# Performance work log

Measured on AMD Instinct MI355X. Metric: run time of the kernel, lower is better.

The kernel has to match this reference:

```python
import jax, jax.numpy as jnp
import numpy as np

B_, S, D_IN, D_OUT = 4, 2048, 4096, 4096
N, RANK, ALPHA = 8, 16, 32
SCALE = ALPHA / RANK


def setup_inputs() -> dict:
    key = jax.random.key(0)
    kx, ka, kb, kw, kbias = jax.random.split(key, 5)
    x = jax.random.normal(kx, (B_, S, D_IN), dtype=jnp.float32)
    # lora_A.weight: [rank, in_features]; lora_B.weight: [out_features, rank]
    lora_A = jax.random.normal(ka, (N, RANK, D_IN), dtype=jnp.float32) * (1.0 / np.sqrt(D_IN))
    lora_B = jax.random.normal(kb, (N, D_OUT, RANK), dtype=jnp.float32) * (1.0 / np.sqrt(RANK))
    W = jax.random.normal(kw, (D_OUT, D_IN), dtype=jnp.float32) * (1.0 / np.sqrt(D_IN))
    bias = jax.random.normal(kbias, (D_OUT,), dtype=jnp.float32) * 0.01
    lora_weights = jnp.full((N,), 1.0 / N, dtype=jnp.float32)  # param_weight init
    return {"x": x, "lora_A": lora_A, "lora_B": lora_B, "W": W,
            "bias": bias, "lora_weights": lora_weights}


def reference(x, lora_A, lora_B, W, bias, lora_weights):
    # Dropout(p=0.01) treated as identity (eval mode) for deterministic reference.
    # low-rank projections for all adapters at once: [n, b, s, r]
    h = jnp.einsum('bsd,nrd->nbsr', x, lora_A)
    # up-projection with per-adapter scale * learned weight fused into B
    coef = (SCALE * lora_weights)[:, None, None]           # [n,1,1]
    lora_out = jnp.einsum('nbsr,nor->bso', h, lora_B * coef)
    base = jnp.einsum('bsd,od->bso', x, W) + bias
    return base + lora_out
```

## Files before the change

### kernel.cpp

```cpp
#include <hip/hip_runtime.h>
#include <hip/hip_bf16.h>
#include <stdint.h>


typedef __attribute__((ext_vector_type(4))) float f32x4;
typedef __attribute__((ext_vector_type(8))) __bf16 bf16x8;
typedef __attribute__((ext_vector_type(8))) unsigned short u16x8;

#define GLOBAL_AS(p) ((const __attribute__((address_space(1))) void*)(p))
#define LDS_AS(p)    ((__attribute__((address_space(3))) void*)(p))

__device__ __forceinline__ ushort f2b(float f) {
    __hip_bfloat16 h = __float2bfloat16(f);
    ushort u;
    __builtin_memcpy(&u, &h, 2);
    return u;
}

__global__ __launch_bounds__(256) void prep_a_kernel(const float* __restrict__ lA,
                                                     ushort* __restrict__ AcatT) {
    __shared__ ushort tile[64][136];
    const int tid = threadIdx.x;
    const int d0 = blockIdx.x * 64;
#pragma unroll
    for (int it = 0; it < 32; ++it) {
        int k = it * 4 + (tid >> 6);
        int dc = tid & 63;
        tile[dc][k] = f2b(lA[(size_t)k * 4096 + d0 + dc]);
    }
    __syncthreads();
#pragma unroll
    for (int it = 0; it < 4; ++it) {
        int g = it * 256 + tid;
        int dc = g >> 4, slot = g & 15;
        u16x8 v;
#pragma unroll
        for (int e = 0; e < 8; ++e) v[e] = tile[dc][slot * 8 + e];
        *reinterpret_cast<u16x8*>(&AcatT[((size_t)(d0 + dc)) * 128 + slot * 8]) = v;
    }
}

__global__ void prep_b_kernel(const float* __restrict__ lB,
                              const float* __restrict__ lw,
                              ushort* __restrict__ Bcat)
{
    int idx = blockIdx.x * 256 + threadIdx.x;
    int o = idx >> 7, k = idx & 127;
    int n = k >> 4, r = k & 15;
    Bcat[idx] = f2b(2.0f * lw[n] * lB[((size_t)n * 4096 + o) * 16 + r]);
}

__global__ void cvtx_kernel(const float* __restrict__ x, ushort* __restrict__ xb) {
    size_t i = ((size_t)blockIdx.x * 256 + threadIdx.x) * 8;
    const float4* xf = (const float4*)(x + i);
    float4 a = xf[0], b = xf[1];
    u16x8 r;
    r[0] = f2b(a.x); r[1] = f2b(a.y); r[2] = f2b(a.z); r[3] = f2b(a.w);
    r[4] = f2b(b.x); r[5] = f2b(b.y); r[6] = f2b(b.z); r[7] = f2b(b.w);
    *reinterpret_cast<u16x8*>(xb + i) = r;
}

template <bool OUT_F32, bool ADD_BIAS, bool ADD_C>
__global__ __launch_bounds__(256) void gemm_bt(
    const ushort* __restrict__ Amat, const ushort* __restrict__ Bmat,
    const float* __restrict__ aux, void* __restrict__ OutP,
    int M, int N, int K)
{
    constexpr int BK = 32;
    __shared__ __align__(16) ushort As[2 * 128 * BK];
    __shared__ __align__(16) ushort Bs[2 * 128 * BK];

    const int tid  = threadIdx.x;
    const int lane = tid & 63;
    const int w    = tid >> 6;
    const int wm   = (w >> 1) * 64;
    const int wn   = (w & 1) * 64;
    const int quad = lane >> 4;
    const int lrow = lane & 15;
    const int m0 = blockIdx.x * 128;
    const int n0 = blockIdx.y * 128;

    const int srow = (w * 2) * 16 + (lane >> 2);
    const int kofs = (lane & 3) * 8;
    const ushort* agp0 = Amat + (size_t)(m0 + srow) * K + kofs;
    const ushort* agp1 = agp0 + (size_t)16 * K;
    const ushort* bgp0 = Bmat + (size_t)(n0 + srow) * K + kofs;
    const ushort* bgp1 = bgp0 + (size_t)16 * K;
    ushort* lA00 = &As[(w * 2) * 512];
    ushort* lA01 = &As[(w * 2 + 1) * 512];
    ushort* lB00 = &Bs[(w * 2) * 512];
    ushort* lB01 = &Bs[(w * 2 + 1) * 512];

    f32x4 acc[4][4] = {};
    const int nK = K >> 6;
    for (int kt = 0; kt < nK; ++kt) {
        __syncthreads();
        __builtin_amdgcn_global_load_lds(GLOBAL_AS(agp0),      LDS_AS(lA00),        16, 0, 0);
        __builtin_amdgcn_global_load_lds(GLOBAL_AS(agp1),      LDS_AS(lA01),        16, 0, 0);
        __builtin_amdgcn_global_load_lds(GLOBAL_AS(agp0 + 32), LDS_AS(lA00 + 4096), 16, 0, 0);
        __builtin_amdgcn_global_load_lds(GLOBAL_AS(agp1 + 32), LDS_AS(lA01 + 4096), 16, 0, 0);
        __builtin_amdgcn_global_load_lds(GLOBAL_AS(bgp0),      LDS_AS(lB00),        16, 0, 0);
        __builtin_amdgcn_global_load_lds(GLOBAL_AS(bgp1),      LDS_AS(lB01),        16, 0, 0);
        __builtin_amdgcn_global_load_lds(GLOBAL_AS(bgp0 + 32), LDS_AS(lB00 + 4096), 16, 0, 0);
        __builtin_amdgcn_global_load_lds(GLOBAL_AS(bgp1 + 32), LDS_AS(lB01 + 4096), 16, 0, 0);
        agp0 += 64; agp1 += 64; bgp0 += 64; bgp1 += 64;
        __syncthreads();

#pragma unroll
        for (int h = 0; h < 2; ++h) {
            const ushort* ab = &As[h * 4096];
            const ushort* bb = &Bs[h * 4096];
            bf16x8 af[4], bfr[4];
#pragma unroll
            for (int i = 0; i < 4; ++i)
                af[i] = *reinterpret_cast<const bf16x8*>(&ab[(wm + i * 16 + lrow) * BK + quad * 8]);
#pragma unroll
            for (int j = 0; j < 4; ++j)
                bfr[j] = *reinterpret_cast<const bf16x8*>(&bb[(wn + j * 16 + lrow) * BK + quad * 8]);
#pragma unroll
            for (int i = 0; i < 4; ++i)
#pragma unroll
                for (int j = 0; j < 4; ++j)
                    acc[i][j] = __builtin_amdgcn_mfma_f32_16x16x32_bf16(af[i], bfr[j], acc[i][j], 0, 0, 0);
        }
    }

#pragma unroll
    for (int i = 0; i < 4; ++i) {
        const int row = m0 + wm + i * 16 + quad * 4;
#pragma unroll
        for (int j = 0; j < 4; ++j) {
            const int col = n0 + wn + j * 16 + lrow;
            float badd = ADD_BIAS ? aux[col] : 0.0f;
#pragma unroll
            for (int v = 0; v < 4; ++v) {
                float val = acc[i][j][v] + badd;
                if (ADD_C) val += aux[(size_t)(row + v) * N + col];
                if (OUT_F32)
                    ((float*)OutP)[(size_t)(row + v) * N + col] = val;
                else
                    ((ushort*)OutP)[(size_t)(row + v) * N + col] = f2b(val);
            }
        }
    }
}

__global__ __launch_bounds__(256) void gemm_af32(
    const float* __restrict__ Af, const ushort* __restrict__ Bmat,
    const float* __restrict__ bias, float* __restrict__ Out,
    int M, int N, int K)
{
    constexpr int BM = 128, BN = 128, BK = 32;
    __shared__ __align__(16) ushort As[BM * BK];
    __shared__ __align__(16) ushort Bs[BN * BK];

    const int tid  = threadIdx.x;
    const int lane = tid & 63;
    const int w    = tid >> 6;
    const int wm   = (w >> 1) * 64;
    const int wn   = (w & 1) * 64;
    const int quad = lane >> 4;
    const int lrow = lane & 15;
    const int m0 = blockIdx.x * BM;
    const int n0 = blockIdx.y * BN;

    const int srow = (w * 2) * 16 + (lane >> 2);
    const int kofs = (lane & 3) * 8;
    const ushort* bgp0 = Bmat + (size_t)(n0 + srow) * K + kofs;
    const ushort* bgp1 = bgp0 + (size_t)16 * K;
    ushort* lB0 = &Bs[(w * 2) * 512];
    ushort* lB1 = &Bs[(w * 2 + 1) * 512];

    f32x4 acc[4][4] = {};
    const int nK = K / BK;
    for (int kt = 0; kt < nK; ++kt) {
        __syncthreads();
        __builtin_amdgcn_global_load_lds(GLOBAL_AS(bgp0), LDS_AS(lB0), 16, 0, 0);
        __builtin_amdgcn_global_load_lds(GLOBAL_AS(bgp1), LDS_AS(lB1), 16, 0, 0);
        bgp0 += BK; bgp1 += BK;
#pragma unroll
        for (int gg = 0; gg < 2; ++gg) {
            int g = tid + gg * 256;
            int row = g >> 2, kc = (g & 3) * 8;
            const float* src = Af + (size_t)(m0 + row) * K + (size_t)kt * BK + kc;
            float4 a = *(const float4*)src;
            float4 b = *(const float4*)(src + 4);
            u16x8 r;
            r[0] = f2b(a.x); r[1] = f2b(a.y); r[2] = f2b(a.z); r[3] = f2b(a.w);
            r[4] = f2b(b.x); r[5] = f2b(b.y); r[6] = f2b(b.z); r[7] = f2b(b.w);
            *reinterpret_cast<u16x8*>(&As[row * BK + kc]) = r;
        }
        __syncthreads();

        bf16x8 af[4], bfr[4];
#pragma unroll
        for (int i = 0; i < 4; ++i)
            af[i] = *reinterpret_cast<const bf16x8*>(&As[(wm + i * 16 + lrow) * BK + quad * 8]);
#pragma unroll
        for (int j = 0; j < 4; ++j)
            bfr[j] = *reinterpret_cast<const bf16x8*>(&Bs[(wn + j * 16 + lrow) * BK + quad * 8]);
#pragma unroll
        for (int i = 0; i < 4; ++i)
#pragma unroll
            for (int j = 0; j < 4; ++j)
                acc[i][j] = __builtin_amdgcn_mfma_f32_16x16x32_bf16(af[i], bfr[j], acc[i][j], 0, 0, 0);
    }

#pragma unroll
    for (int i = 0; i < 4; ++i) {
        const int row = m0 + wm + i * 16 + quad * 4;
#pragma unroll
        for (int j = 0; j < 4; ++j) {
            const int col = n0 + wn + j * 16 + lrow;
            float badd = bias[col];
#pragma unroll
            for (int v = 0; v < 4; ++v)
                Out[(size_t)(row + v) * N + col] = acc[i][j][v] + badd;
        }
    }
}

__global__ void naive_kernel(const float* __restrict__ x, const float* __restrict__ lA,
                             const float* __restrict__ lB, const float* __restrict__ W,
                             const float* __restrict__ bias, const float* __restrict__ lw,
                             float* __restrict__ out)
{
    __shared__ float xs[4096];
    __shared__ float h[128];
    const int m = blockIdx.x;
    for (int d = threadIdx.x; d < 4096; d += 256)
        xs[d] = x[(size_t)m * 4096 + d];
    __syncthreads();
    for (int k = threadIdx.x; k < 128; k += 256) {
        const float* arow = lA + (size_t)k * 4096;
        float s = 0.f;
        for (int d = 0; d < 4096; ++d) s += xs[d] * arow[d];
        h[k] = s;
    }
    __syncthreads();
    for (int o = threadIdx.x; o < 4096; o += 256) {
        const float* wrow = W + (size_t)o * 4096;
        float s = bias[o];
        for (int d = 0; d < 4096; ++d) s += xs[d] * wrow[d];
        for (int n = 0; n < 8; ++n) {
            const float* brow = lB + ((size_t)n * 4096 + o) * 16;
            float t = 0.f;
            for (int r = 0; r < 16; ++r) t += h[n * 16 + r] * brow[r];
            s += 2.0f * lw[n] * t;
        }
        out[(size_t)m * 4096 + o] = s;
    }
}

extern "C" void kernel_launch(void* const* d_in, const int* in_sizes, int n_in,
                              void* d_out, int out_size, void* d_ws, size_t ws_size,
                              hipStream_t stream)
{
    const float* x    = (const float*)d_in[0];
    const float* lA   = (const float*)d_in[1];
    const float* lB   = (const float*)d_in[2];
    const float* W    = (const float*)d_in[3];
    const float* bias = (const float*)d_in[4];
    const float* lw   = (const float*)d_in[5];
    float* out = (float*)d_out;

    ushort* Bcat  = (ushort*)d_ws;
    ushort* AcatT = Bcat + (size_t)4096 * 128;
    ushort* Weff  = AcatT + (size_t)4096 * 128;
    ushort* xb    = Weff + (size_t)4096 * 4096;
    const size_t need_t2 = (2 * (size_t)4096 * 128 + (size_t)4096 * 4096) * 2;
    const size_t need_t1 = need_t2 + (size_t)8192 * 4096 * 2;

    if (ws_size >= need_t2) {
        prep_a_kernel<<<64, 256, 0, stream>>>(lA, AcatT);
        prep_b_kernel<<<2048, 256, 0, stream>>>(lB, lw, Bcat);
        gemm_bt<false, false, true><<<dim3(32, 32), 256, 0, stream>>>(
            Bcat, AcatT, W, Weff, 4096, 4096, 128);
        if (ws_size >= need_t1) {
            cvtx_kernel<<<16384, 256, 0, stream>>>(x, xb);
            gemm_bt<true, true, false><<<dim3(64, 32), 256, 0, stream>>>(
                xb, Weff, bias, out, 8192, 4096, 4096);
        } else {
            gemm_af32<<<dim3(64, 32), 256, 0, stream>>>(
                x, Weff, bias, out, 8192, 4096, 4096);
        }
    } else {
        naive_kernel<<<8192, 256, 0, stream>>>(x, lA, lB, W, bias, lw, out);
    }
}
```

Before: 651.5 us.

## Replace main bf16 GEMM with 256x256-tile pipelined kernel using direct global-to-LDS loads

Swaps the 128x128 gemm_bt used for the dominant x·Weff product for a new 512-thread kernel computing 256x256 output tiles. It double-buffers LDS via global_load_lds, swizzles LDS columns to avoid bank conflicts, interleaves quarter-tile loads with MFMA groups using barriers and setprio, and remaps block ids for L2 locality. The larger tile raises arithmetic intensity and overlaps memory with compute, at the cost of heavy register use (128 accumulators) and hand-tuned waitcnt logic that depends on the exact dimensions.

```diff
diff --git a/kernel.cpp b/kernel.cpp
--- a/kernel.cpp
+++ b/kernel.cpp
@@ -145,6 +145,156 @@
     }
 }
 
+__global__ __launch_bounds__(512, 2) void gemm256_bias(
+    const ushort* __restrict__ Amat, const ushort* __restrict__ Bmat,
+    const float* __restrict__ bias, float* __restrict__ Out,
+    int M, int N, int K)
+{
+    __shared__ __align__(16) ushort As[2][2][128 * 64];
+    __shared__ __align__(16) ushort Bs[2][2][128 * 64];
+
+    const int tid  = threadIdx.x;
+    const int l    = tid & 63;
+    const int w    = tid >> 6;
+    const int wr   = w >> 2;
+    const int wc   = w & 3;
+    const int quad = l >> 4;
+    const int lrow = l & 15;
+
+    const int nbn = N >> 8;
+    const int cpx = gridDim.x >> 3;
+    int id = ((int)blockIdx.x & 7) * cpx + ((int)blockIdx.x >> 3);
+    const int m0 = (id / nbn) * 256;
+    const int n0 = (id % nbn) * 256;
+
+    const int cOff = ((l & 7) * 8) ^ (((l >> 5) & 1) << 4);
+    const ushort* aBase = Amat + (size_t)(m0 + (w * 2) * 8 + (l >> 3)) * K + cOff;
+    const ushort* bBase = Bmat + (size_t)(n0 + (w * 2) * 8 + (l >> 3)) * K + cOff;
+    const int dC = 8 * K;
+    const int dH = 128 * K;
+    const int st0 = w * 1024;
+    const int st1 = w * 1024 + 512;
+
+    const int aRow0 = wr * 64 + lrow;
+    const int bCol0 = wc * 32 + lrow;
+    const int kqf = ((lrow >> 2) & 1) << 4;
+    const int kq0 = (quad * 8) ^ kqf;
+    const int kq1 = (32 + quad * 8) ^ kqf;
+
+    f32x4 acc[8][4] = {};
+    bf16x8 af[4][2], bf[2][2];
+
+    const int nT = K >> 6;
+
+#define GLDS(gp, lp) __builtin_amdgcn_global_load_lds(GLOBAL_AS(gp), LDS_AS(lp), 16, 0, 0)
+
+#define LOAD_AF(cur_, half_) do { \
+    af[0][0] = *reinterpret_cast<const bf16x8*>(&As[cur_][half_][(aRow0 +  0) * 64 + kq0]); \
+    af[0][1] = *reinterpret_cast<const bf16x8*>(&As[cur_][half_][(aRow0 +  0) * 64 + kq1]); \
+    af[1][0] = *reinterpret_cast<const bf16x8*>(&As[cur_][half_][(aRow0 + 16) * 64 + kq0]); \
+    af[1][1] = *reinterpret_cast<const bf16x8*>(&As[cur_][half_][(aRow0 + 16) * 64 + kq1]); \
+    af[2][0] = *reinterpret_cast<const bf16x8*>(&As[cur_][half_][(aRow0 + 32) * 64 + kq0]); \
+    af[2][1] = *reinterpret_cast<const bf16x8*>(&As[cur_][half_][(aRow0 + 32) * 64 + kq1]); \
+    af[3][0] = *reinterpret_cast<const bf16x8*>(&As[cur_][half_][(aRow0 + 48) * 64 + kq0]); \
+    af[3][1] = *reinterpret_cast<const bf16x8*>(&As[cur_][half_][(aRow0 + 48) * 64 + kq1]); \
+} while (0)
+
+#define LOAD_BF(cur_, half_) do { \
+    bf[0][0] = *reinterpret_cast<const bf16x8*>(&Bs[cur_][half_][(bCol0 +  0) * 64 + kq0]); \
+    bf[0][1] = *reinterpret_cast<const bf16x8*>(&Bs[cur_][half_][(bCol0 +  0) * 64 + kq1]); \
+    bf[1][0] = *reinterpret_cast<const bf16x8*>(&Bs[cur_][half_][(bCol0 + 16) * 64 + kq0]); \
+    bf[1][1] = *reinterpret_cast<const bf16x8*>(&Bs[cur_][half_][(bCol0 + 16) * 64 + kq1]); \
+} while (0)
+
+#define MFMA1(qm_, qn_, i_, j_, kh_) \
+    acc[(qm_) * 4 + (i_)][(qn_) * 2 + (j_)] = __builtin_amdgcn_mfma_f32_16x16x32_bf16( \
+        af[i_][kh_], bf[j_][kh_], acc[(qm_) * 4 + (i_)][(qn_) * 2 + (j_)], 0, 0, 0)
+
+#define MFMA_QUAD(qm_, qn_) do { \
+    MFMA1(qm_,qn_,0,0,0); MFMA1(qm_,qn_,0,1,0); MFMA1(qm_,qn_,1,0,0); MFMA1(qm_,qn_,1,1,0); \
+    MFMA1(qm_,qn_,2,0,0); MFMA1(qm_,qn_,2,1,0); MFMA1(qm_,qn_,3,0,0); MFMA1(qm_,qn_,3,1,0); \
+    MFMA1(qm_,qn_,0,0,1); MFMA1(qm_,qn_,0,1,1); MFMA1(qm_,qn_,1,0,1); MFMA1(qm_,qn_,1,1,1); \
+    MFMA1(qm_,qn_,2,0,1); MFMA1(qm_,qn_,2,1,1); MFMA1(qm_,qn_,3,0,1); MFMA1(qm_,qn_,3,1,1); \
+} while (0)
+
+#define BAR_MID() do { \
+    asm volatile("" ::: "memory"); \
+    __builtin_amdgcn_s_barrier(); \
+    __builtin_amdgcn_sched_barrier(0); \
+    asm volatile("s_waitcnt lgkmcnt(0)" ::: "memory"); \
+    __builtin_amdgcn_sched_barrier(0); \
+    __builtin_amdgcn_s_setprio(1); \
+} while (0)
+
+#define BAR_END() do { \
+    __builtin_amdgcn_s_setprio(0); \
+    asm volatile("" ::: "memory"); \
+    __builtin_amdgcn_s_barrier(); \
+    __builtin_amdgcn_sched_barrier(0); \
+} while (0)
+
+#define VGUARD() asm volatile("s_waitcnt vmcnt(4)" ::: "memory")
+
+#define TILE_STEP(cur_, nxt_, tt_) do { \
+    const int ks = ((tt_) + 1) << 6; \
+    const bool doSt = ((tt_) + 1) < nT; \
+     \
+    LOAD_AF(cur_, 0); LOAD_BF(cur_, 0); \
+    if (doSt) { GLDS(aBase + ks, &As[nxt_][0][st0]); GLDS(aBase + dC + ks, &As[nxt_][0][st1]); } \
+    BAR_MID(); MFMA_QUAD(0, 0); VGUARD(); BAR_END(); \
+     \
+    LOAD_BF(cur_, 1); \
+    if (doSt) { GLDS(bBase + ks, &Bs[nxt_][0][st0]); GLDS(bBase + dC + ks, &Bs[nxt_][0][st1]); } \
+    BAR_MID(); MFMA_QUAD(0, 1); VGUARD(); BAR_END(); \
+     \
+    LOAD_AF(cur_, 1); \
+    if (doSt) { GLDS(bBase + dH + ks, &Bs[nxt_][1][st0]); GLDS(bBase + dH + dC + ks, &Bs[nxt_][1][st1]); } \
+    BAR_MID(); MFMA_QUAD(1, 1); BAR_END(); \
+     \
+    LOAD_BF(cur_, 0); \
+    if (doSt) { GLDS(aBase + dH + ks, &As[nxt_][1][st0]); GLDS(aBase + dH + dC + ks, &As[nxt_][1][st1]); } \
+    BAR_MID(); MFMA_QUAD(1, 0); VGUARD(); BAR_END(); \
+} while (0)
+
+    GLDS(aBase,           &As[0][0][st0]); GLDS(aBase + dC,      &As[0][0][st1]);
+    GLDS(bBase,           &Bs[0][0][st0]); GLDS(bBase + dC,      &Bs[0][0][st1]);
+    GLDS(bBase + dH,      &Bs[0][1][st0]); GLDS(bBase + dH + dC, &Bs[0][1][st1]);
+    GLDS(aBase + dH,      &As[0][1][st0]); GLDS(aBase + dH + dC, &As[0][1][st1]);
+    asm volatile("s_waitcnt vmcnt(4)" ::: "memory");
+    asm volatile("" ::: "memory");
+    __builtin_amdgcn_s_barrier();
+    __builtin_amdgcn_sched_barrier(0);
+
+#pragma unroll 1
+    for (int t = 0; t < nT; t += 2) {
+        TILE_STEP(0, 1, t);
+        TILE_STEP(1, 0, t + 1);
+    }
+
+#pragma unroll
+    for (int i = 0; i < 8; ++i) {
+        const int row = m0 + (i >> 2) * 128 + wr * 64 + (i & 3) * 16 + quad * 4;
+#pragma unroll
+        for (int j = 0; j < 4; ++j) {
+            const int col = n0 + (j >> 1) * 128 + wc * 32 + (j & 1) * 16 + lrow;
+            const float badd = bias[col];
+#pragma unroll
+            for (int v = 0; v < 4; ++v)
+                Out[(size_t)(row + v) * N + col] = acc[i][j][v] + badd;
+        }
+    }
+
+#undef GLDS
+#undef LOAD_AF
+#undef LOAD_BF
+#undef MFMA1
+#undef MFMA_QUAD
+#undef BAR_MID
+#undef BAR_END
+#undef VGUARD
+#undef TILE_STEP
+}
+
 __global__ __launch_bounds__(256) void gemm_af32(
     const float* __restrict__ Af, const ushort* __restrict__ Bmat,
     const float* __restrict__ bias, float* __restrict__ Out,
@@ -278,7 +428,7 @@
             Bcat, AcatT, W, Weff, 4096, 4096, 128);
         if (ws_size >= need_t1) {
             cvtx_kernel<<<16384, 256, 0, stream>>>(x, xb);
-            gemm_bt<true, true, false><<<dim3(64, 32), 256, 0, stream>>>(
+            gemm256_bias<<<dim3(512), 512, 0, stream>>>(
                 xb, Weff, bias, out, 8192, 4096, 4096);
         } else {
             gemm_af32<<<dim3(64, 32), 256, 0, stream>>>(
```

Result: faster. 562.8 us (-13.6%).
